# Kernel tuning notes

Hardware: AMD Instinct MI355X
Metric: run time of the kernel (lower is better)

Reference implementation:

```python
import jax, jax.numpy as jnp
import numpy as np

NUM_USERS, NUM_ITEMS, D = 100000, 200000, 128
B, LLEN, SLEN = 4096, 200, 50
NEG = -1e9


def setup_inputs() -> dict:
    key = jax.random.key(0)
    ks = jax.random.split(key, 10)
    w_range = float(np.sqrt(3.0 / D))
    return {
        "user_table": 0.01 * jax.random.normal(ks[0], (NUM_USERS, D), dtype=jnp.float32),
        "item_table": 0.01 * jax.random.normal(ks[1], (NUM_ITEMS, D), dtype=jnp.float32),
        "W1": jax.random.uniform(ks[2], (2 * D, 16), minval=-w_range, maxval=w_range, dtype=jnp.float32),
        "b1": jnp.zeros((16,), dtype=jnp.float32),
        "W2": jax.random.uniform(ks[3], (16, 1), minval=-w_range, maxval=w_range, dtype=jnp.float32),
        "b2": jnp.zeros((1,), dtype=jnp.float32),
        "user_inputs": jax.random.randint(ks[4], (B,), 0, NUM_USERS, dtype=jnp.int64) if jax.config.jax_enable_x64 else jax.random.randint(ks[4], (B,), 0, NUM_USERS, dtype=jnp.int32),
        "L_inputs": jax.random.randint(ks[5], (B, LLEN), 0, NUM_ITEMS, dtype=jnp.int32),
        "S_inputs": jax.random.randint(ks[6], (B, SLEN), 0, NUM_ITEMS, dtype=jnp.int32),
        "item_inputs": jax.random.randint(ks[7], (B,), 0, NUM_ITEMS, dtype=jnp.int32),
    }


def reference(user_table, item_table, W1, b1, W2, b2,
              user_inputs, L_inputs, S_inputs, item_inputs):
    def att_logits(x):  # x: [..., 2D] -> [...]
        h = jax.nn.relu(x @ W1 + b1)
        return (h @ W2 + b2)[..., 0]

    def masked_softmax(logits, mask):  # softmax over last axis restricted to mask
        logits = jnp.where(mask, logits, NEG)
        return jax.nn.softmax(logits, axis=-1)

    u_emb = user_table[user_inputs]                      # [B, D]

    # ---- long-term attention over L history ----
    L_mask = L_inputs >= 0                               # [B, L]
    L_idx = jnp.where(L_mask, L_inputs, 0)
    L_emb = item_table[L_idx]                            # [B, L, D]
    uL = jnp.concatenate([jnp.broadcast_to(u_emb[:, None, :], L_emb.shape), L_emb], axis=-1)  # [B, L, 2D]
    w1 = masked_softmax(att_logits(uL), L_mask)          # [B, L]
    u_long = jnp.einsum('bl,bld->bd', w1, L_emb)         # [B, D]

    # ---- short-term attention over [u_long] + S (L assumed nonempty) ----
    S_mask = S_inputs >= 0                               # [B, S]
    S_idx = jnp.where(S_mask, S_inputs, 0)
    S_emb = item_table[S_idx]                            # [B, S, D]
    seq = jnp.concatenate([u_long[:, None, :], S_emb], axis=1)   # [B, 1+S, D]
    seq_mask = jnp.concatenate([jnp.ones((seq.shape[0], 1), dtype=bool), S_mask], axis=1)
    uSeq = jnp.concatenate([jnp.broadcast_to(u_emb[:, None, :], seq.shape), seq], axis=-1)  # [B, 1+S, 2D]
    w2 = masked_softmax(att_logits(uSeq), seq_mask)      # [B, 1+S]
    user_hybrid = jnp.einsum('bs,bsd->bd', w2, seq)      # [B, D]

    # ---- score: bmm([B,1,D], [B,D,1]) -> [B,1,1] ----
    item_emb = item_table[item_inputs]                   # [B, D]
    score = jnp.sum(user_hybrid * item_emb, axis=-1)[:, None, None]
    return score
```

## Files before the change

kernel.cpp:

```cpp
#include <hip/hip_runtime.h>
#include <math.h>

#define D 128
#define LLEN 200
#define SLEN 50
#define ESTR 132

typedef __attribute__((ext_vector_type(8))) short short8;
typedef __attribute__((ext_vector_type(4))) float f32x4;

__device__ __forceinline__ unsigned short f2bf(float f) {
  unsigned int u = __float_as_uint(f);
  return (unsigned short)((u + 0x7FFFu + ((u >> 16) & 1u)) >> 16);
}

__device__ __forceinline__ float wave_red_sum(float v) {
#pragma unroll
  for (int m = 32; m >= 1; m >>= 1) v += __shfl_xor(v, m, 64);
  return v;
}
__device__ __forceinline__ float block_sum(float v, float* red) {
  v = wave_red_sum(v);
  if ((threadIdx.x & 63) == 0) red[threadIdx.x >> 6] = v;
  __syncthreads();
  v = red[0] + red[1] + red[2] + red[3];
  __syncthreads();
  return v;
}

#define GATHER_L(dst, IT, BASE)                        \
  do {                                                 \
    int s_ = tid + (IT);                               \
    int gid_ = rows1[(BASE) + (s_ >> 5)];              \
    if (gid_ < 0) gid_ = 0;                            \
    dst = it4[(size_t)gid_ * 32 + (s_ & 31)];          \
  } while (0)

#define GATHER_S(dst, IT)                              \
  do {                                                 \
    int s_ = tid + (IT);                               \
    int gid_ = rowsS[s_ >> 5];                         \
    if (gid_ < 0) gid_ = 0;                            \
    dst = it4[(size_t)gid_ * 32 + (s_ & 31)];          \
  } while (0)

#define STORE_L(src, IT)                                                     \
  do {                                                                       \
    int s_ = tid + (IT);                                                     \
    reinterpret_cast<float4*>(&ebuf[(s_ >> 5) * ESTR])[s_ & 31] = src;       \
  } while (0)

#define STORE_S(src, IT)                                                     \
  do {                                                                       \
    int s_ = tid + (IT);                                                     \
    reinterpret_cast<float4*>(&ebuf[((s_ >> 5) + 1) * ESTR])[s_ & 31] = src; \
  } while (0)

#define FMA4(WL, P, ACC)                \
  do {                                  \
    ACC.x = fmaf((WL), P.x, ACC.x);     \
    ACC.y = fmaf((WL), P.y, ACC.y);     \
    ACC.z = fmaf((WL), P.z, ACC.z);     \
  } while (0);                          \
  ACC.w = fmaf((WL), P.w, ACC.w)

#define PACK8(DST, FA, FB)                                 \
  do {                                                     \
    DST[0] = (short)f2bf(FA.x); DST[1] = (short)f2bf(FA.y);\
    DST[2] = (short)f2bf(FA.z); DST[3] = (short)f2bf(FA.w);\
    DST[4] = (short)f2bf(FB.x); DST[5] = (short)f2bf(FB.y);\
    DST[6] = (short)f2bf(FB.z); DST[7] = (short)f2bf(FB.w);\
  } while (0)

template <int MODE>
__device__ __forceinline__ void mfma_logits(
    const float* eb, short8 Bf0, short8 Bf1, short8 Bf2, short8 Bf3,
    int w, int lane, float upart_j, float w2j, float b2v,
    const int* rowm, int nvalid, float* w_sh, float& pacc) {
  const int row = 16 * w + (lane & 15);
  const float4* ap4 =
      reinterpret_cast<const float4*>(&eb[row * ESTR + 8 * (lane >> 4)]);
  float4 f0 = ap4[0], f1 = ap4[1];
  float4 f2 = ap4[8], f3 = ap4[9];
  float4 f4 = ap4[16], f5 = ap4[17];
  float4 f6 = ap4[24], f7 = ap4[25];
  short8 a0, a1, a2, a3;
  PACK8(a0, f0, f1); PACK8(a1, f2, f3); PACK8(a2, f4, f5); PACK8(a3, f6, f7);
  f32x4 acc = {0.f, 0.f, 0.f, 0.f};
  acc = __builtin_amdgcn_mfma_f32_16x16x32_bf16(a0, Bf0, acc, 0, 0, 0);
  acc = __builtin_amdgcn_mfma_f32_16x16x32_bf16(a1, Bf1, acc, 0, 0, 0);
  acc = __builtin_amdgcn_mfma_f32_16x16x32_bf16(a2, Bf2, acc, 0, 0, 0);
  acc = __builtin_amdgcn_mfma_f32_16x16x32_bf16(a3, Bf3, acc, 0, 0, 0);
  float v0 = fmaxf(upart_j + acc[0], 0.f) * w2j;
  float v1 = fmaxf(upart_j + acc[1], 0.f) * w2j;
  float v2 = fmaxf(upart_j + acc[2], 0.f) * w2j;
  float v3 = fmaxf(upart_j + acc[3], 0.f) * w2j;
#pragma unroll
  for (int m = 1; m <= 8; m <<= 1) {
    v0 += __shfl_xor(v0, m, 64);
    v1 += __shfl_xor(v1, m, 64);
    v2 += __shfl_xor(v2, m, 64);
    v3 += __shfl_xor(v3, m, 64);
  }
  if ((lane & 15) == 0) {
    const int it0 = 16 * w + 4 * (lane >> 4);
    float p0, p1, p2, p3;
    if (MODE == 0) {
      p0 = (it0 + 0 < nvalid && rowm[it0 + 0] >= 0) ? expf(v0 + b2v) : 0.f;
      p1 = (it0 + 1 < nvalid && rowm[it0 + 1] >= 0) ? expf(v1 + b2v) : 0.f;
      p2 = (it0 + 2 < nvalid && rowm[it0 + 2] >= 0) ? expf(v2 + b2v) : 0.f;
      p3 = (it0 + 3 < nvalid && rowm[it0 + 3] >= 0) ? expf(v3 + b2v) : 0.f;
    } else {
      p0 = (it0 == 0) ? expf(v0 + b2v)
                      : ((it0 < nvalid && rowm[it0 - 1] >= 0) ? expf(v0 + b2v) : 0.f);
      p1 = (it0 + 1 < nvalid && rowm[it0 + 0] >= 0) ? expf(v1 + b2v) : 0.f;
      p2 = (it0 + 2 < nvalid && rowm[it0 + 1] >= 0) ? expf(v2 + b2v) : 0.f;
      p3 = (it0 + 3 < nvalid && rowm[it0 + 2] >= 0) ? expf(v3 + b2v) : 0.f;
    }
    float4 pv;
    pv.x = p0; pv.y = p1; pv.z = p2; pv.w = p3;
    reinterpret_cast<float4*>(w_sh)[it0 >> 2] = pv;
    pacc += p0 + p1 + p2 + p3;
  }
}

__global__ void __launch_bounds__(256, 4) din_kernel(
    const float* __restrict__ user_table, const float* __restrict__ item_table,
    const float* __restrict__ W1, const float* __restrict__ b1,
    const float* __restrict__ W2, const float* __restrict__ b2,
    const int* __restrict__ user_inputs, const int* __restrict__ L_inputs,
    const int* __restrict__ S_inputs, const int* __restrict__ item_inputs,
    float* __restrict__ out) {
  __shared__ __align__(16) float ebuf[64 * ESTR];
  __shared__ __align__(16) float w_sh[64];
  __shared__ int rows1[LLEN];
  __shared__ int rowsS[SLEN];
  __shared__ float upart_sh[16];
  __shared__ float red_sh[4];

  const int b = blockIdx.x;
  const int tid = threadIdx.x;
  const int lane = tid & 63;
  const int w = __builtin_amdgcn_readfirstlane(tid >> 6);
  const int col4 = tid & 31;
  const int grp = tid >> 5;
  const float4* it4 = reinterpret_cast<const float4*>(item_table);

  float* u_sh = &ebuf[0];
  float* part = &ebuf[128];
  if (tid < D) u_sh[tid] = user_table[(size_t)user_inputs[b] * D + tid];
  const float item_f =
      (tid < D) ? item_table[(size_t)item_inputs[b] * D + tid] : 0.f;
  if (tid < LLEN) rows1[tid] = L_inputs[(size_t)b * LLEN + tid];
  if (tid < SLEN) rowsS[tid] = S_inputs[(size_t)b * SLEN + tid];
  __syncthreads();

  float4 P0, P1, P2, P3, P4, P5, P6, P7;
  GATHER_L(P0, 0, 0);    GATHER_L(P1, 256, 0);  GATHER_L(P2, 512, 0);
  GATHER_L(P3, 768, 0);  GATHER_L(P4, 1024, 0); GATHER_L(P5, 1280, 0);
  GATHER_L(P6, 1536, 0); GATHER_L(P7, 1792, 0);

  short8 Bf0, Bf1, Bf2, Bf3;
  {
    const int j = lane & 15, ko = lane >> 4;
    const float* wp = &W1[(size_t)(128 + 8 * ko) * 16 + j];
#pragma unroll
    for (int t = 0; t < 8; ++t) {
      Bf0[t] = (short)f2bf(wp[t * 16]);
      Bf1[t] = (short)f2bf(wp[(32 + t) * 16]);
      Bf2[t] = (short)f2bf(wp[(64 + t) * 16]);
      Bf3[t] = (short)f2bf(wp[(96 + t) * 16]);
    }
  }

  {
    int j = tid & 15, g = tid >> 4;
    float p = 0.f;
#pragma unroll
    for (int t = 0; t < 8; ++t) {
      int d = g * 8 + t;
      p = fmaf(u_sh[d], W1[d * 16 + j], p);
    }
    part[tid] = p;
  }
  __syncthreads();
  if (tid < 16) {
    float s = b1[tid];
#pragma unroll
    for (int g = 0; g < 16; ++g) s += part[g * 16 + tid];
    upart_sh[tid] = s;
  }
  __syncthreads();

  const float b2v = b2[0];
  const float upart_j = upart_sh[lane & 15];
  const float w2j = W2[lane & 15];

  float pacc = 0.f;
  float4 uacc = make_float4(0.f, 0.f, 0.f, 0.f);
  float wl;

#pragma unroll 1
  for (int c = 0; c < 3; ++c) {
    const int base = c * 64;
    STORE_L(P0, 0);    STORE_L(P1, 256);  STORE_L(P2, 512);  STORE_L(P3, 768);
    STORE_L(P4, 1024); STORE_L(P5, 1280); STORE_L(P6, 1536); STORE_L(P7, 1792);
    __syncthreads();
    mfma_logits<0>(ebuf, Bf0, Bf1, Bf2, Bf3, w, lane, upart_j, w2j, b2v,
                   rows1 + base, 64, w_sh, pacc);
    __syncthreads();
    if (c < 2) {
      GATHER_L(P0, 0, base + 64);    GATHER_L(P1, 256, base + 64);
      GATHER_L(P2, 512, base + 64);  GATHER_L(P3, 768, base + 64);
      GATHER_L(P4, 1024, base + 64); GATHER_L(P5, 1280, base + 64);
      GATHER_L(P6, 1536, base + 64); GATHER_L(P7, 1792, base + 64);
    } else {
      GATHER_L(P0, 0, 192);
      GATHER_S(P1, 0);    GATHER_S(P2, 256);  GATHER_S(P3, 512);
      GATHER_S(P4, 768);  GATHER_S(P5, 1024); GATHER_S(P6, 1280);
      if (tid < 64) GATHER_S(P7, 1536);
    }
#pragma unroll
    for (int i = 0; i < 8; ++i) {
      int l = grp + 8 * i;
      wl = w_sh[l];
      const float4 e = reinterpret_cast<const float4*>(&ebuf[l * ESTR])[col4];
      FMA4(wl, e, uacc);
    }
    __syncthreads();
  }

  STORE_L(P0, 0);
  __syncthreads();
  if (w == 0)
    mfma_logits<0>(ebuf, Bf0, Bf1, Bf2, Bf3, w, lane, upart_j, w2j, b2v,
                   rows1 + 192, 8, w_sh, pacc);
  __syncthreads();
  wl = w_sh[grp];
  {
    const float4 e = reinterpret_cast<const float4*>(&ebuf[grp * ESTR])[col4];
    FMA4(wl, e, uacc);
  }

  const float invS1 = 1.f / block_sum(pacc, red_sh);
  uacc.x += __shfl_xor(uacc.x, 32, 64);
  uacc.y += __shfl_xor(uacc.y, 32, 64);
  uacc.z += __shfl_xor(uacc.z, 32, 64);
  uacc.w += __shfl_xor(uacc.w, 32, 64);
  float* scr = &ebuf[52 * ESTR];
  if (lane < 32) reinterpret_cast<float4*>(scr)[(w << 5) + lane] = uacc;
  STORE_S(P1, 0);    STORE_S(P2, 256);  STORE_S(P3, 512);
  STORE_S(P4, 768);  STORE_S(P5, 1024); STORE_S(P6, 1280);
  if (tid < 64) STORE_S(P7, 1536);
  __syncthreads();
  if (tid < D) {
    float s = scr[tid] + scr[128 + tid] + scr[256 + tid] + scr[384 + tid];
    ebuf[tid] = s * invS1;
  }
  __syncthreads();

  float pacc2 = 0.f;
  mfma_logits<1>(ebuf, Bf0, Bf1, Bf2, Bf3, w, lane, upart_j, w2j, b2v,
                 rowsS, 51, w_sh, pacc2);
  const float invS2 = 1.f / block_sum(pacc2, red_sh);

  float4 uacc2 = make_float4(0.f, 0.f, 0.f, 0.f);
#pragma unroll
  for (int i = 0; i < 6; ++i) {
    int l = grp + 8 * i;
    wl = w_sh[l];
    const float4 e = reinterpret_cast<const float4*>(&ebuf[l * ESTR])[col4];
    FMA4(wl, e, uacc2);
  }
  if (grp < 3) {
    int l = 48 + grp;
    wl = w_sh[l];
    const float4 e = reinterpret_cast<const float4*>(&ebuf[l * ESTR])[col4];
    FMA4(wl, e, uacc2);
  }

  uacc2.x += __shfl_xor(uacc2.x, 32, 64);
  uacc2.y += __shfl_xor(uacc2.y, 32, 64);
  uacc2.z += __shfl_xor(uacc2.z, 32, 64);
  uacc2.w += __shfl_xor(uacc2.w, 32, 64);
  if (lane < 32) reinterpret_cast<float4*>(scr)[(w << 5) + lane] = uacc2;
  __syncthreads();

  float sv = 0.f;
  if (tid < D) {
    float s = scr[tid] + scr[128 + tid] + scr[256 + tid] + scr[384 + tid];
    sv = s * invS2 * item_f;
  }
  float tot = block_sum(sv, red_sh);
  if (tid == 0) out[b] = tot;
}

extern "C" void kernel_launch(void* const* d_in, const int* in_sizes, int n_in,
                              void* d_out, int out_size, void* d_ws, size_t ws_size,
                              hipStream_t stream) {
  const float* user_table = (const float*)d_in[0];
  const float* item_table = (const float*)d_in[1];
  const float* W1 = (const float*)d_in[2];
  const float* b1 = (const float*)d_in[3];
  const float* W2 = (const float*)d_in[4];
  const float* b2 = (const float*)d_in[5];
  const int* user_inputs = (const int*)d_in[6];
  const int* L_inputs = (const int*)d_in[7];
  const int* S_inputs = (const int*)d_in[8];
  const int* item_inputs = (const int*)d_in[9];
  float* out = (float*)d_out;

  const int B = in_sizes[6];
  din_kernel<<<B, 256, 0, stream>>>(user_table, item_table, W1, b1, W2, b2,
                                    user_inputs, L_inputs, S_inputs, item_inputs,
                                    out);
}
```

Baseline: 268.8 us.

## Gather embeddings directly into LDS via global_load_lds with XOR swizzle

Replaces the register-staged gather (global load into registers, then store to shared memory) with direct global-to-LDS async loads, using an XOR swizzle on the column index in place of row padding to avoid bank conflicts. The W1 item-half weights are transposed into bf16 in LDS instead of being held as per-lane register fragments, and the user-part projection is reduced with shuffles rather than through shared memory. This frees registers, which may help occupancy, and drops the per-element LDS store instructions. The cost is that the prefetch now happens after the accumulation step instead of overlapping with it, which may expose gather latency, and the swizzled addressing must be correct for every reader.

```diff
diff --git a/kernel.cpp b/kernel.cpp
--- a/kernel.cpp
+++ b/kernel.cpp
@@ -1,13 +1,15 @@
 #include <hip/hip_runtime.h>
 #include <math.h>
+#include <stdint.h>
 
 #define D 128
 #define LLEN 200
 #define SLEN 50
-#define ESTR 132
 
 typedef __attribute__((ext_vector_type(8))) short short8;
 typedef __attribute__((ext_vector_type(4))) float f32x4;
+typedef __attribute__((address_space(3))) unsigned int lds_uint;
+typedef __attribute__((address_space(1))) unsigned int gbl_uint;
 
 __device__ __forceinline__ unsigned short f2bf(float f) {
   unsigned int u = __float_as_uint(f);
@@ -28,32 +30,18 @@
   return v;
 }
 
-#define GATHER_L(dst, IT, BASE)                        \
-  do {                                                 \
-    int s_ = tid + (IT);                               \
-    int gid_ = rows1[(BASE) + (s_ >> 5)];              \
-    if (gid_ < 0) gid_ = 0;                            \
-    dst = it4[(size_t)gid_ * 32 + (s_ & 31)];          \
-  } while (0)
-
-#define GATHER_S(dst, IT)                              \
-  do {                                                 \
-    int s_ = tid + (IT);                               \
-    int gid_ = rowsS[s_ >> 5];                         \
-    if (gid_ < 0) gid_ = 0;                            \
-    dst = it4[(size_t)gid_ * 32 + (s_ & 31)];          \
-  } while (0)
-
-#define STORE_L(src, IT)                                                     \
-  do {                                                                       \
-    int s_ = tid + (IT);                                                     \
-    reinterpret_cast<float4*>(&ebuf[(s_ >> 5) * ESTR])[s_ & 31] = src;       \
-  } while (0)
-
-#define STORE_S(src, IT)                                                     \
-  do {                                                                       \
-    int s_ = tid + (IT);                                                     \
-    reinterpret_cast<float4*>(&ebuf[((s_ >> 5) + 1) * ESTR])[s_ & 31] = src; \
+#define STAGE(ROWARR, RBASE, IT, ROFF)                                        \
+  do {                                                                        \
+    const int s_ = tid + (IT) * 256;                                          \
+    const int rr_ = (s_ >> 5) + (ROFF);                                       \
+    int gid_ = ROWARR[(RBASE) + (s_ >> 5)];                                   \
+    if (gid_ < 0) gid_ = 0;                                                   \
+    const float4* src_ = &it4[(size_t)gid_ * 32 + ((s_ & 31) ^ (rr_ & 7))];   \
+    __builtin_amdgcn_global_load_lds(                                         \
+        (const gbl_uint*)(uintptr_t)src_,                                     \
+        (lds_uint*)(uintptr_t)(&ebuf[((tid & 192) + (IT) * 256) * 4 +         \
+                                     (ROFF) * 128]),                          \
+        16, 0, 0);                                                            \
   } while (0)
 
 #define FMA4(WL, P, ACC)                \
@@ -64,33 +52,30 @@
   } while (0);                          \
   ACC.w = fmaf((WL), P.w, ACC.w)
 
-#define PACK8(DST, FA, FB)                                 \
-  do {                                                     \
-    DST[0] = (short)f2bf(FA.x); DST[1] = (short)f2bf(FA.y);\
-    DST[2] = (short)f2bf(FA.z); DST[3] = (short)f2bf(FA.w);\
-    DST[4] = (short)f2bf(FB.x); DST[5] = (short)f2bf(FB.y);\
-    DST[6] = (short)f2bf(FB.z); DST[7] = (short)f2bf(FB.w);\
-  } while (0)
-
 template <int MODE>
 __device__ __forceinline__ void mfma_logits(
-    const float* eb, short8 Bf0, short8 Bf1, short8 Bf2, short8 Bf3,
+    const float* eb, const unsigned short* w1t,
     int w, int lane, float upart_j, float w2j, float b2v,
     const int* rowm, int nvalid, float* w_sh, float& pacc) {
-  const int row = 16 * w + (lane & 15);
-  const float4* ap4 =
-      reinterpret_cast<const float4*>(&eb[row * ESTR + 8 * (lane >> 4)]);
-  float4 f0 = ap4[0], f1 = ap4[1];
-  float4 f2 = ap4[8], f3 = ap4[9];
-  float4 f4 = ap4[16], f5 = ap4[17];
-  float4 f6 = ap4[24], f7 = ap4[25];
-  short8 a0, a1, a2, a3;
-  PACK8(a0, f0, f1); PACK8(a1, f2, f3); PACK8(a2, f4, f5); PACK8(a3, f6, f7);
+  const int jj = lane & 15, ko = lane >> 4;
+  const int x = lane & 7;
+  const int q0 = (2 * ko) ^ x, q1 = q0 ^ 1;
+  const int row = 16 * w + jj;
+  const float4* rp = reinterpret_cast<const float4*>(&eb[row * 128]);
+  const unsigned short* wp = &w1t[jj * 136 + 8 * ko];
   f32x4 acc = {0.f, 0.f, 0.f, 0.f};
-  acc = __builtin_amdgcn_mfma_f32_16x16x32_bf16(a0, Bf0, acc, 0, 0, 0);
-  acc = __builtin_amdgcn_mfma_f32_16x16x32_bf16(a1, Bf1, acc, 0, 0, 0);
-  acc = __builtin_amdgcn_mfma_f32_16x16x32_bf16(a2, Bf2, acc, 0, 0, 0);
-  acc = __builtin_amdgcn_mfma_f32_16x16x32_bf16(a3, Bf3, acc, 0, 0, 0);
+#pragma unroll
+  for (int s = 0; s < 4; ++s) {
+    float4 fa = rp[q0 + 8 * s];
+    float4 fb = rp[q1 + 8 * s];
+    short8 bfrag = *reinterpret_cast<const short8*>(wp + 32 * s);
+    short8 afrag;
+    afrag[0] = (short)f2bf(fa.x); afrag[1] = (short)f2bf(fa.y);
+    afrag[2] = (short)f2bf(fa.z); afrag[3] = (short)f2bf(fa.w);
+    afrag[4] = (short)f2bf(fb.x); afrag[5] = (short)f2bf(fb.y);
+    afrag[6] = (short)f2bf(fb.z); afrag[7] = (short)f2bf(fb.w);
+    acc = __builtin_amdgcn_mfma_f32_16x16x32_bf16(afrag, bfrag, acc, 0, 0, 0);
+  }
   float v0 = fmaxf(upart_j + acc[0], 0.f) * w2j;
   float v1 = fmaxf(upart_j + acc[1], 0.f) * w2j;
   float v2 = fmaxf(upart_j + acc[2], 0.f) * w2j;
@@ -131,7 +116,8 @@
     const int* __restrict__ user_inputs, const int* __restrict__ L_inputs,
     const int* __restrict__ S_inputs, const int* __restrict__ item_inputs,
     float* __restrict__ out) {
-  __shared__ __align__(16) float ebuf[64 * ESTR];
+  __shared__ __align__(16) float ebuf[64 * 128];
+  __shared__ __align__(16) unsigned short w1t_sh[16 * 136];
   __shared__ __align__(16) float w_sh[64];
   __shared__ int rows1[LLEN];
   __shared__ int rowsS[SLEN];
@@ -146,50 +132,38 @@
   const int grp = tid >> 5;
   const float4* it4 = reinterpret_cast<const float4*>(item_table);
 
-  float* u_sh = &ebuf[0];
-  float* part = &ebuf[128];
-  if (tid < D) u_sh[tid] = user_table[(size_t)user_inputs[b] * D + tid];
+  const int urow = user_inputs[b];
   const float item_f =
       (tid < D) ? item_table[(size_t)item_inputs[b] * D + tid] : 0.f;
   if (tid < LLEN) rows1[tid] = L_inputs[(size_t)b * LLEN + tid];
   if (tid < SLEN) rowsS[tid] = S_inputs[(size_t)b * SLEN + tid];
   __syncthreads();
 
-  float4 P0, P1, P2, P3, P4, P5, P6, P7;
-  GATHER_L(P0, 0, 0);    GATHER_L(P1, 256, 0);  GATHER_L(P2, 512, 0);
-  GATHER_L(P3, 768, 0);  GATHER_L(P4, 1024, 0); GATHER_L(P5, 1280, 0);
-  GATHER_L(P6, 1536, 0); GATHER_L(P7, 1792, 0);
-
-  short8 Bf0, Bf1, Bf2, Bf3;
+  STAGE(rows1, 0, 0, 0); STAGE(rows1, 0, 1, 0); STAGE(rows1, 0, 2, 0);
+  STAGE(rows1, 0, 3, 0); STAGE(rows1, 0, 4, 0); STAGE(rows1, 0, 5, 0);
+  STAGE(rows1, 0, 6, 0); STAGE(rows1, 0, 7, 0);
+
   {
-    const int j = lane & 15, ko = lane >> 4;
-    const float* wp = &W1[(size_t)(128 + 8 * ko) * 16 + j];
-#pragma unroll
-    for (int t = 0; t < 8; ++t) {
-      Bf0[t] = (short)f2bf(wp[t * 16]);
-      Bf1[t] = (short)f2bf(wp[(32 + t) * 16]);
-      Bf2[t] = (short)f2bf(wp[(64 + t) * 16]);
-      Bf3[t] = (short)f2bf(wp[(96 + t) * 16]);
-    }
-  }
-
-  {
-    int j = tid & 15, g = tid >> 4;
+    const int j = tid & 15, g = tid >> 4;
+    const float* up = &user_table[(size_t)urow * D + 8 * g];
+    const float* wp = &W1[(size_t)(8 * g) * 16 + j];
     float p = 0.f;
 #pragma unroll
-    for (int t = 0; t < 8; ++t) {
-      int d = g * 8 + t;
-      p = fmaf(u_sh[d], W1[d * 16 + j], p);
-    }
-    part[tid] = p;
-  }
-  __syncthreads();
-  if (tid < 16) {
-    float s = b1[tid];
-#pragma unroll
-    for (int g = 0; g < 16; ++g) s += part[g * 16 + tid];
-    upart_sh[tid] = s;
-  }
+    for (int t = 0; t < 8; ++t) p = fmaf(up[t], wp[t * 16], p);
+    p += __shfl_xor(p, 16, 64);
+    p += __shfl_xor(p, 32, 64);
+    if (lane < 16) w_sh[w * 16 + lane] = p;
+  }
+#pragma unroll
+  for (int i = 0; i < 8; ++i) {
+    int idx = tid + i * 256;
+    int j = idx & 15, k = idx >> 4;
+    w1t_sh[j * 136 + k] = f2bf(W1[(size_t)(128 + k) * 16 + j]);
+  }
+  __syncthreads();
+  if (tid < 16)
+    upart_sh[tid] = b1[tid] + w_sh[tid] + w_sh[16 + tid] + w_sh[32 + tid] +
+                    w_sh[48 + tid];
   __syncthreads();
 
   const float b2v = b2[0];
@@ -198,60 +172,53 @@
 
   float pacc = 0.f;
   float4 uacc = make_float4(0.f, 0.f, 0.f, 0.f);
-  float wl;
 
 #pragma unroll 1
   for (int c = 0; c < 3; ++c) {
-    const int base = c * 64;
-    STORE_L(P0, 0);    STORE_L(P1, 256);  STORE_L(P2, 512);  STORE_L(P3, 768);
-    STORE_L(P4, 1024); STORE_L(P5, 1280); STORE_L(P6, 1536); STORE_L(P7, 1792);
+    mfma_logits<0>(ebuf, w1t_sh, w, lane, upart_j, w2j, b2v,
+                   rows1 + c * 64, 64, w_sh, pacc);
     __syncthreads();
-    mfma_logits<0>(ebuf, Bf0, Bf1, Bf2, Bf3, w, lane, upart_j, w2j, b2v,
-                   rows1 + base, 64, w_sh, pacc);
-    __syncthreads();
-    if (c < 2) {
-      GATHER_L(P0, 0, base + 64);    GATHER_L(P1, 256, base + 64);
-      GATHER_L(P2, 512, base + 64);  GATHER_L(P3, 768, base + 64);
-      GATHER_L(P4, 1024, base + 64); GATHER_L(P5, 1280, base + 64);
-      GATHER_L(P6, 1536, base + 64); GATHER_L(P7, 1792, base + 64);
-    } else {
-      GATHER_L(P0, 0, 192);
-      GATHER_S(P1, 0);    GATHER_S(P2, 256);  GATHER_S(P3, 512);
-      GATHER_S(P4, 768);  GATHER_S(P5, 1024); GATHER_S(P6, 1280);
-      if (tid < 64) GATHER_S(P7, 1536);
-    }
 #pragma unroll
     for (int i = 0; i < 8; ++i) {
       int l = grp + 8 * i;
-      wl = w_sh[l];
-      const float4 e = reinterpret_cast<const float4*>(&ebuf[l * ESTR])[col4];
+      float wl = w_sh[l];
+      const float4 e = reinterpret_cast<const float4*>(&ebuf[l * 128])[col4 ^ grp];
       FMA4(wl, e, uacc);
     }
     __syncthreads();
-  }
-
-  STORE_L(P0, 0);
-  __syncthreads();
+    if (c < 2) {
+      const int nb = c * 64 + 64;
+      STAGE(rows1, nb, 0, 0); STAGE(rows1, nb, 1, 0); STAGE(rows1, nb, 2, 0);
+      STAGE(rows1, nb, 3, 0); STAGE(rows1, nb, 4, 0); STAGE(rows1, nb, 5, 0);
+      STAGE(rows1, nb, 6, 0); STAGE(rows1, nb, 7, 0);
+    } else {
+      STAGE(rows1, 192, 0, 0);
+      STAGE(rowsS, 0, 1, 1); STAGE(rowsS, 0, 2, 1); STAGE(rowsS, 0, 3, 1);
+      STAGE(rowsS, 0, 4, 1); STAGE(rowsS, 0, 5, 1);
+      if (tid < 64) STAGE(rowsS, 0, 6, 1);
+    }
+    __syncthreads();
+  }
+
   if (w == 0)
-    mfma_logits<0>(ebuf, Bf0, Bf1, Bf2, Bf3, w, lane, upart_j, w2j, b2v,
+    mfma_logits<0>(ebuf, w1t_sh, w, lane, upart_j, w2j, b2v,
                    rows1 + 192, 8, w_sh, pacc);
   __syncthreads();
-  wl = w_sh[grp];
   {
-    const float4 e = reinterpret_cast<const float4*>(&ebuf[grp * ESTR])[col4];
+    float wl = w_sh[grp];
+    const float4 e = reinterpret_cast<const float4*>(&ebuf[grp * 128])[col4 ^ grp];
     FMA4(wl, e, uacc);
   }
+  __syncthreads();
+  STAGE(rowsS, 0, 0, 1);
 
   const float invS1 = 1.f / block_sum(pacc, red_sh);
   uacc.x += __shfl_xor(uacc.x, 32, 64);
   uacc.y += __shfl_xor(uacc.y, 32, 64);
   uacc.z += __shfl_xor(uacc.z, 32, 64);
   uacc.w += __shfl_xor(uacc.w, 32, 64);
-  float* scr = &ebuf[52 * ESTR];
+  float* scr = &ebuf[52 * 128];
   if (lane < 32) reinterpret_cast<float4*>(scr)[(w << 5) + lane] = uacc;
-  STORE_S(P1, 0);    STORE_S(P2, 256);  STORE_S(P3, 512);
-  STORE_S(P4, 768);  STORE_S(P5, 1024); STORE_S(P6, 1280);
-  if (tid < 64) STORE_S(P7, 1536);
   __syncthreads();
   if (tid < D) {
     float s = scr[tid] + scr[128 + tid] + scr[256 + tid] + scr[384 + tid];
@@ -260,7 +227,7 @@
   __syncthreads();
 
   float pacc2 = 0.f;
-  mfma_logits<1>(ebuf, Bf0, Bf1, Bf2, Bf3, w, lane, upart_j, w2j, b2v,
+  mfma_logits<1>(ebuf, w1t_sh, w, lane, upart_j, w2j, b2v,
                  rowsS, 51, w_sh, pacc2);
   const float invS2 = 1.f / block_sum(pacc2, red_sh);
 
@@ -268,14 +235,14 @@
 #pragma unroll
   for (int i = 0; i < 6; ++i) {
     int l = grp + 8 * i;
-    wl = w_sh[l];
-    const float4 e = reinterpret_cast<const float4*>(&ebuf[l * ESTR])[col4];
+    float wl = w_sh[l];
+    const float4 e = reinterpret_cast<const float4*>(&ebuf[l * 128])[col4 ^ grp];
     FMA4(wl, e, uacc2);
   }
   if (grp < 3) {
     int l = 48 + grp;
-    wl = w_sh[l];
-    const float4 e = reinterpret_cast<const float4*>(&ebuf[l * ESTR])[col4];
+    float wl = w_sh[l];
+    const float4 e = reinterpret_cast<const float4*>(&ebuf[l * 128])[col4 ^ grp];
     FMA4(wl, e, uacc2);
   }
 
```

Measured after the change: 253.6 us. 5.7% less time.
